# Kernel optimization log

Hardware: AMD Instinct MI355X
Metric: run time of the kernel (lower is better)

## Reference

```python
import jax, jax.numpy as jnp
import numpy as np

DIM = 1024
B, S = 4, 2048


def setup_inputs() -> dict:
    key = jax.random.key(0)
    kx, kq, kk, kv, ko = jax.random.split(key, 5)
    scale = 1.0 / np.sqrt(DIM)
    return {
        "x": jax.random.normal(kx, (B, S, DIM), dtype=jnp.float32),
        "wq": jax.random.normal(kq, (DIM, DIM), dtype=jnp.float32) * scale,
        "wk": jax.random.normal(kk, (DIM, DIM), dtype=jnp.float32) * scale,
        "wv": jax.random.normal(kv, (DIM, DIM), dtype=jnp.float32) * scale,
        "wo": jax.random.normal(ko, (DIM, DIM), dtype=jnp.float32) * scale,
    }


def reference(x, wq, wk, wv, wo):
    # nn.Linear(y) = y @ W.T ; weights stored [out, in]
    q = jnp.einsum("bsd,ed->bse", x, wq)
    k = jnp.einsum("bsd,ed->bse", x, wk)
    v = jnp.einsum("bsd,ed->bse", x, wv)
    # NOTE: no head split in original module; full-dim attention, scale = sqrt(dim)
    scores = jnp.einsum("bqd,bkd->bqk", q, k) / jnp.sqrt(jnp.float32(DIM))
    attn = jax.nn.softmax(scores, axis=-1)
    ctx = jnp.einsum("bqk,bkd->bqd", attn, v)
    return jnp.einsum("bsd,ed->bse", ctx, wo)
```

## Files before the change

### kernel.cpp

```cpp
#include <hip/hip_runtime.h>
#include <hip/hip_bf16.h>
#include <cstdio>
#include <cstdint>


typedef __attribute__((ext_vector_type(8))) short short8;
typedef __attribute__((ext_vector_type(4))) float f32x4;

#define AS1(p) ((const __attribute__((address_space(1))) void*)(p))
#define AS3(p) ((__attribute__((address_space(3))) void*)(p))

__device__ __forceinline__ unsigned short f2bf(float f) {
  union { float f; uint32_t u; } c; c.f = f;
  uint32_t u = c.u + 0x7fffu + ((c.u >> 16) & 1u);
  return (unsigned short)(u >> 16);
}

__global__ void cvt_f32_bf16(const float* __restrict__ in,
                             unsigned short* __restrict__ out, int n4) {
  int i = blockIdx.x * 256 + threadIdx.x;
  if (i >= n4) return;
  float4 v = ((const float4*)in)[i];
  ushort4 o;
  o.x = f2bf(v.x); o.y = f2bf(v.y); o.z = f2bf(v.z); o.w = f2bf(v.w);
  ((ushort4*)out)[i] = o;
}

__global__ void cvt_w4(const float* __restrict__ a, const float* __restrict__ b,
                       const float* __restrict__ c, const float* __restrict__ d,
                       unsigned short* __restrict__ out) {
  const float* s = (blockIdx.y == 0) ? a : (blockIdx.y == 1) ? b
                 : (blockIdx.y == 2) ? c : d;
  int i = blockIdx.x * 256 + threadIdx.x;
  float4 v = ((const float4*)s)[i];
  ushort4 o;
  o.x = f2bf(v.x); o.y = f2bf(v.y); o.z = f2bf(v.z); o.w = f2bf(v.w);
  ((ushort4*)(out + (size_t)blockIdx.y * 1048576))[i] = o;
}

__global__ void transpose_bf16(const unsigned short* __restrict__ V,
                               unsigned short* __restrict__ Vt) {
  __shared__ unsigned short tile[64][72];
  const int b = blockIdx.z;
  const unsigned short* v = V + (size_t)b * 2048 * 1024;
  unsigned short* vt = Vt + (size_t)b * 1024 * 2048;
  const int d0 = blockIdx.x * 64, s0 = blockIdx.y * 64;
  const int t = threadIdx.x;
#pragma unroll
  for (int it = 0; it < 16; ++it) {
    int idx = it * 256 + t, r = idx >> 6, c = idx & 63;
    tile[r][c] = v[(size_t)(s0 + r) * 1024 + d0 + c];
  }
  __syncthreads();
#pragma unroll
  for (int it = 0; it < 16; ++it) {
    int idx = it * 256 + t, r = idx >> 6, c = idx & 63;
    vt[(size_t)(d0 + r) * 2048 + s0 + c] = tile[c][r];
  }
}

__global__ void softmax_rows(const float* __restrict__ S,
                             unsigned short* __restrict__ P) {
  const size_t row = blockIdx.x;
  const float* s = S + row * 2048;
  const int t = threadIdx.x, l = t & 63, w = t >> 6;
  float4 v0 = ((const float4*)s)[t * 2];
  float4 v1 = ((const float4*)s)[t * 2 + 1];
  float x[8] = {v0.x, v0.y, v0.z, v0.w, v1.x, v1.y, v1.z, v1.w};
  float m = x[0];
#pragma unroll
  for (int j = 1; j < 8; ++j) m = fmaxf(m, x[j]);
#pragma unroll
  for (int d = 32; d; d >>= 1) m = fmaxf(m, __shfl_xor(m, d));
  __shared__ float rm[4], rs[4];
  if (l == 0) rm[w] = m;
  __syncthreads();
  m = fmaxf(fmaxf(rm[0], rm[1]), fmaxf(rm[2], rm[3]));
  float e[8], sum = 0.f;
#pragma unroll
  for (int j = 0; j < 8; ++j) { e[j] = __expf(x[j] - m); sum += e[j]; }
#pragma unroll
  for (int d = 32; d; d >>= 1) sum += __shfl_xor(sum, d);
  if (l == 0) rs[w] = sum;
  __syncthreads();
  float inv = 1.0f / (rs[0] + rs[1] + rs[2] + rs[3]);
  short8 o;
#pragma unroll
  for (int j = 0; j < 8; ++j) o[j] = (short)f2bf(e[j] * inv);
  *(short8*)(P + row * 2048 + t * 8) = o;
}

__device__ __forceinline__ void store_out(float* p, float v) { *p = v; }
__device__ __forceinline__ void store_out(unsigned short* p, float v) { *p = f2bf(v); }

template <typename OutT>
__global__ __launch_bounds__(512, 2) void gemm8p(
    const unsigned short* __restrict__ A, const unsigned short* __restrict__ B,
    OutT* __restrict__ C, int lda, int ldb, int ldc, int nT,
    long long aStride, long long bStride, long long cStride, float scale) {
  __shared__ unsigned short lds[65536];
  const int l = threadIdx.x & 63, w = threadIdx.x >> 6;
  const int wr = w >> 2, wc = w & 3;

  const int gx = gridDim.x, gy = gridDim.y;
  int f = blockIdx.x + gx * (blockIdx.y + gy * blockIdx.z);
  int nwg = gx * gy * gridDim.z;
  int work = ((nwg & 7) == 0) ? ((f & 7) * (nwg >> 3) + (f >> 3)) : f;
  const int bx = work % gx;
  int rem = work / gx;
  const int by = rem % gy, bz = rem / gy;
  const long long r0 = (long long)by * 256, c0 = (long long)bx * 256;
  A += (size_t)bz * aStride;
  B += (size_t)bz * bStride;
  C += (size_t)bz * cStride;

  const unsigned short* aS = A + (size_t)(r0 + w * 16 + (l & 15)) * lda + (l >> 4) * 8;
  const unsigned short* bS = B + (size_t)(c0 + w * 16 + (l & 15)) * ldb + (l >> 4) * 8;
  const size_t a128 = (size_t)128 * lda, b128 = (size_t)128 * ldb;
  char* const ldsc = (char*)lds;
  const int dstW = (w * 2) << 10;

#define STAGE_A(t_, h_)                                                        \
  do {                                                                         \
    const unsigned short* s_ = aS + ((h_) ? a128 : 0) + (t_) * 64;             \
    char* d_ = ldsc + (((t_) & 1) << 16) + ((h_) << 14) + dstW;                \
    __builtin_amdgcn_global_load_lds(AS1(s_), AS3(d_), 16, 0, 0);              \
    __builtin_amdgcn_global_load_lds(AS1(s_ + 32), AS3(d_ + 1024), 16, 0, 0);  \
  } while (0)
#define STAGE_B(t_, h_)                                                        \
  do {                                                                         \
    const unsigned short* s_ = bS + ((h_) ? b128 : 0) + (t_) * 64;             \
    char* d_ = ldsc + (((t_) & 1) << 16) + 32768 + ((h_) << 14) + dstW;        \
    __builtin_amdgcn_global_load_lds(AS1(s_), AS3(d_), 16, 0, 0);              \
    __builtin_amdgcn_global_load_lds(AS1(s_ + 32), AS3(d_ + 1024), 16, 0, 0);  \
  } while (0)

  short8 a[8], b0[4], b1[4];
  f32x4 acc[8][4] = {};

  const int aBase = wr << 14;
  const int bBase = 32768 + ((wc >> 1) << 14);
  const int bFr = (wc & 1) * 4;
  const int loff = l * 16;

#define LDA_SET(s_, qm_)                                                       \
  _Pragma("unroll") for (int m2 = 0; m2 < 4; ++m2)                             \
  _Pragma("unroll") for (int kk = 0; kk < 2; ++kk)                             \
      a[m2 * 2 + kk] = *(const short8*)(ldsc + ((s_) << 16) + aBase +          \
                                        ((((qm_) * 4 + m2) * 2 + kk) << 10) + loff);
#define LDB_SET(s_, qn_, dst_)                                                 \
  _Pragma("unroll") for (int n2 = 0; n2 < 2; ++n2)                             \
  _Pragma("unroll") for (int kk = 0; kk < 2; ++kk)                             \
      dst_[n2 * 2 + kk] = *(const short8*)(ldsc + ((s_) << 16) + bBase +       \
                                           (((bFr + (qn_) * 2 + n2) * 2 + kk) << 10) + loff);
#define MFMA_Q(qm_, qn_, bset_)                                                \
  __builtin_amdgcn_s_setprio(1);                                               \
  _Pragma("unroll") for (int m2 = 0; m2 < 4; ++m2)                             \
  _Pragma("unroll") for (int n2 = 0; n2 < 2; ++n2)                             \
  _Pragma("unroll") for (int kk = 0; kk < 2; ++kk)                             \
      acc[(qm_) * 4 + m2][(qn_) * 2 + n2] =                                    \
          __builtin_amdgcn_mfma_f32_16x16x32_bf16(                             \
              a[m2 * 2 + kk], bset_[n2 * 2 + kk],                              \
              acc[(qm_) * 4 + m2][(qn_) * 2 + n2], 0, 0, 0);                   \
  __builtin_amdgcn_s_setprio(0);
#define BAR() asm volatile("s_barrier" ::: "memory")
#define LGKM0() asm volatile("s_waitcnt lgkmcnt(0)" ::: "memory")
#define VMC(n_) asm volatile("s_waitcnt vmcnt(" #n_ ")" ::: "memory")

  STAGE_B(0, 0); STAGE_B(0, 1); STAGE_A(0, 0); STAGE_A(0, 1);
  STAGE_B(1, 0); STAGE_B(1, 1); STAGE_A(1, 0);
  VMC(6); BAR();

  const int nI = nT >> 1;
  for (int i = 0; i < nI; ++i) {
    const int t0 = 2 * i;
    const bool last = (i == nI - 1);
    LDA_SET(0, 0); LDB_SET(0, 0, b0);
    STAGE_A(t0 + 1, 1);
    BAR(); LGKM0(); MFMA_Q(0, 0, b0); BAR();
    LDB_SET(0, 1, b1);
    BAR(); LGKM0(); MFMA_Q(0, 1, b1); BAR();
    LDA_SET(0, 1);
    if (!last) STAGE_B(t0 + 2, 0);
    BAR(); LGKM0(); MFMA_Q(1, 1, b1); BAR();
    if (!last) { STAGE_B(t0 + 2, 1); VMC(4); } else { VMC(0); }
    BAR(); MFMA_Q(1, 0, b0); BAR();
    LDA_SET(1, 0); LDB_SET(1, 0, b0);
    if (!last) STAGE_A(t0 + 2, 0);
    BAR(); LGKM0(); MFMA_Q(0, 0, b0); BAR();
    LDB_SET(1, 1, b1);
    if (!last) STAGE_A(t0 + 2, 1);
    BAR(); LGKM0(); MFMA_Q(0, 1, b1); BAR();
    LDA_SET(1, 1);
    if (!last) STAGE_B(t0 + 3, 0);
    BAR(); LGKM0(); MFMA_Q(1, 1, b1); BAR();
    if (!last) { STAGE_B(t0 + 3, 1); STAGE_A(t0 + 3, 0); VMC(6); }
    BAR(); MFMA_Q(1, 0, b0); BAR();
  }
#undef STAGE_A
#undef STAGE_B
#undef LDA_SET
#undef LDB_SET
#undef MFMA_Q

  const int cr = (l >> 4) * 4, cc = l & 15;
  const long long rowb = r0 + wr * 128, colb = c0 + wc * 64;
#pragma unroll
  for (int m = 0; m < 8; ++m)
#pragma unroll
    for (int n = 0; n < 4; ++n) {
      long long col = colb + n * 16 + cc;
#pragma unroll
      for (int i2 = 0; i2 < 4; ++i2) {
        long long row = rowb + m * 16 + cr + i2;
        store_out(&C[row * ldc + col], acc[m][n][i2] * scale);
      }
    }
}

static const size_t OFF_XB  = 0;
static const size_t OFF_WQ  = 16777216;
static const size_t OFF_WK  = 18874368;
static const size_t OFF_WV  = 20971520;
static const size_t OFF_WO  = 23068672;
static const size_t OFF_Q   = 25165824;
static const size_t OFF_K   = 41943040;
static const size_t OFF_V   = 58720256;
static const size_t OFF_VT  = 75497472;
static const size_t OFF_SC  = 92274688;
static const size_t OFF_P   = 159383552;
static const size_t OFF_CTX = 192937984;
static const size_t WS_NEED = 209715200;

extern "C" void kernel_launch(void* const* d_in, const int* in_sizes, int n_in,
                              void* d_out, int out_size, void* d_ws, size_t ws_size,
                              hipStream_t stream) {
  const float* x  = (const float*)d_in[0];
  const float* wq = (const float*)d_in[1];
  const float* wk = (const float*)d_in[2];
  const float* wv = (const float*)d_in[3];
  const float* wo = (const float*)d_in[4];
  float* out = (float*)d_out;

  if (ws_size < WS_NEED) {
    fprintf(stderr, "kernel_launch: ws_size=%zu < needed %zu\n", ws_size, WS_NEED);
    return;
  }
  char* ws = (char*)d_ws;
  unsigned short* xb  = (unsigned short*)(ws + OFF_XB);
  unsigned short* wqb = (unsigned short*)(ws + OFF_WQ);
  unsigned short* wob = (unsigned short*)(ws + OFF_WO);
  unsigned short* Qb  = (unsigned short*)(ws + OFF_Q);
  unsigned short* Kb  = (unsigned short*)(ws + OFF_K);
  unsigned short* Vb  = (unsigned short*)(ws + OFF_V);
  unsigned short* Vt  = (unsigned short*)(ws + OFF_VT);
  float*          Sc  = (float*)(ws + OFF_SC);
  unsigned short* Pb  = (unsigned short*)(ws + OFF_P);
  unsigned short* Cx  = (unsigned short*)(ws + OFF_CTX);

  cvt_f32_bf16<<<8192, 256, 0, stream>>>(x, xb, 2097152);
  cvt_w4<<<dim3(1024, 4, 1), 256, 0, stream>>>(wq, wk, wv, wo, wqb);

  gemm8p<unsigned short><<<dim3(4, 32, 3), 512, 0, stream>>>(
      xb, wqb, Qb, 1024, 1024, 1024, 16, 0, 1048576LL, 8388608LL, 1.0f);

  transpose_bf16<<<dim3(16, 32, 4), 256, 0, stream>>>(Vb, Vt);

  gemm8p<float><<<dim3(8, 8, 4), 512, 0, stream>>>(
      Qb, Kb, Sc, 1024, 1024, 2048, 16,
      2097152LL, 2097152LL, 4194304LL, 0.03125f);

  softmax_rows<<<8192, 256, 0, stream>>>(Sc, Pb);

  gemm8p<unsigned short><<<dim3(4, 8, 4), 512, 0, stream>>>(
      Pb, Vt, Cx, 2048, 2048, 1024, 32,
      4194304LL, 2097152LL, 2097152LL, 1.0f);

  gemm8p<float><<<dim3(4, 32, 1), 512, 0, stream>>>(
      Cx, wob, out, 1024, 1024, 1024, 16, 0, 0, 0, 1.0f);
}
```

Measured before the change: 342.9 us.

## Restructure GEMM main loop with register double-buffered LDS reads and whole-tile staging

Rewrites the GEMM inner loop so LDS fragment reads for the next quarter-tile are issued before the current MFMA block, using separate even/odd A register sets and partial lgkmcnt waits instead of full waits. Global-to-LDS staging now loads a whole K-tile (A and B, both halves) at once into alternating slots, with fewer barriers per quarter. Sched barriers pin the ordering. This aims to hide LDS read latency behind MFMAs, at the cost of more registers and coarser global prefetch granularity.

```diff
diff --git a/kernel.cpp b/kernel.cpp
--- a/kernel.cpp
+++ b/kernel.cpp
@@ -94,7 +94,7 @@
 __device__ __forceinline__ void store_out(unsigned short* p, float v) { *p = f2bf(v); }
 
 template <typename OutT>
-__global__ __launch_bounds__(512, 2) void gemm8p(
+__global__ __launch_bounds__(512, 2) void gemm8w(
     const unsigned short* __restrict__ A, const unsigned short* __restrict__ B,
     OutT* __restrict__ C, int lda, int ldb, int ldc, int nT,
     long long aStride, long long bStride, long long cStride, float scale) {
@@ -119,89 +119,86 @@
   const size_t a128 = (size_t)128 * lda, b128 = (size_t)128 * ldb;
   char* const ldsc = (char*)lds;
   const int dstW = (w * 2) << 10;
-
-#define STAGE_A(t_, h_)                                                        \
-  do {                                                                         \
-    const unsigned short* s_ = aS + ((h_) ? a128 : 0) + (t_) * 64;             \
-    char* d_ = ldsc + (((t_) & 1) << 16) + ((h_) << 14) + dstW;                \
-    __builtin_amdgcn_global_load_lds(AS1(s_), AS3(d_), 16, 0, 0);              \
-    __builtin_amdgcn_global_load_lds(AS1(s_ + 32), AS3(d_ + 1024), 16, 0, 0);  \
-  } while (0)
-#define STAGE_B(t_, h_)                                                        \
-  do {                                                                         \
-    const unsigned short* s_ = bS + ((h_) ? b128 : 0) + (t_) * 64;             \
-    char* d_ = ldsc + (((t_) & 1) << 16) + 32768 + ((h_) << 14) + dstW;        \
-    __builtin_amdgcn_global_load_lds(AS1(s_), AS3(d_), 16, 0, 0);              \
-    __builtin_amdgcn_global_load_lds(AS1(s_ + 32), AS3(d_ + 1024), 16, 0, 0);  \
-  } while (0)
-
-  short8 a[8], b0[4], b1[4];
-  f32x4 acc[8][4] = {};
-
   const int aBase = wr << 14;
   const int bBase = 32768 + ((wc >> 1) << 14);
   const int bFr = (wc & 1) * 4;
   const int loff = l * 16;
 
-#define LDA_SET(s_, qm_)                                                       \
-  _Pragma("unroll") for (int m2 = 0; m2 < 4; ++m2)                             \
+#define STG(slot_, koff_)                                                      \
+  do {                                                                         \
+    const unsigned short* sa_ = aS + (koff_);                                  \
+    const unsigned short* sb_ = bS + (koff_);                                  \
+    char* da_ = ldsc + ((slot_) << 16) + dstW;                                 \
+    char* db_ = ldsc + ((slot_) << 16) + 32768 + dstW;                         \
+    __builtin_amdgcn_global_load_lds(AS1(sa_), AS3(da_), 16, 0, 0);            \
+    __builtin_amdgcn_global_load_lds(AS1(sa_ + 32), AS3(da_ + 1024), 16, 0, 0);\
+    __builtin_amdgcn_global_load_lds(AS1(sa_ + a128), AS3(da_ + 16384), 16, 0, 0);\
+    __builtin_amdgcn_global_load_lds(AS1(sa_ + a128 + 32), AS3(da_ + 17408), 16, 0, 0);\
+    __builtin_amdgcn_global_load_lds(AS1(sb_), AS3(db_), 16, 0, 0);            \
+    __builtin_amdgcn_global_load_lds(AS1(sb_ + 32), AS3(db_ + 1024), 16, 0, 0);\
+    __builtin_amdgcn_global_load_lds(AS1(sb_ + b128), AS3(db_ + 16384), 16, 0, 0);\
+    __builtin_amdgcn_global_load_lds(AS1(sb_ + b128 + 32), AS3(db_ + 17408), 16, 0, 0);\
+  } while (0)
+
+#define RDA(dst_, slot_, hs_)                                                  \
+  _Pragma("unroll") for (int f2 = 0; f2 < 4; ++f2)                             \
   _Pragma("unroll") for (int kk = 0; kk < 2; ++kk)                             \
-      a[m2 * 2 + kk] = *(const short8*)(ldsc + ((s_) << 16) + aBase +          \
-                                        ((((qm_) * 4 + m2) * 2 + kk) << 10) + loff);
-#define LDB_SET(s_, qn_, dst_)                                                 \
+      dst_[f2 * 2 + kk] = *(const short8*)(ldsc + ((slot_) << 16) + aBase +    \
+                                           ((((hs_) * 4 + f2) * 2 + kk) << 10) + loff);
+#define RDB(dst_, slot_, qn_)                                                  \
   _Pragma("unroll") for (int n2 = 0; n2 < 2; ++n2)                             \
   _Pragma("unroll") for (int kk = 0; kk < 2; ++kk)                             \
-      dst_[n2 * 2 + kk] = *(const short8*)(ldsc + ((s_) << 16) + bBase +       \
+      dst_[n2 * 2 + kk] = *(const short8*)(ldsc + ((slot_) << 16) + bBase +    \
                                            (((bFr + (qn_) * 2 + n2) * 2 + kk) << 10) + loff);
-#define MFMA_Q(qm_, qn_, bset_)                                                \
+#define MQ(ar_, mo_, br_, no_)                                                 \
   __builtin_amdgcn_s_setprio(1);                                               \
   _Pragma("unroll") for (int m2 = 0; m2 < 4; ++m2)                             \
   _Pragma("unroll") for (int n2 = 0; n2 < 2; ++n2)                             \
   _Pragma("unroll") for (int kk = 0; kk < 2; ++kk)                             \
-      acc[(qm_) * 4 + m2][(qn_) * 2 + n2] =                                    \
-          __builtin_amdgcn_mfma_f32_16x16x32_bf16(                             \
-              a[m2 * 2 + kk], bset_[n2 * 2 + kk],                              \
-              acc[(qm_) * 4 + m2][(qn_) * 2 + n2], 0, 0, 0);                   \
+      acc[(mo_) + m2][(no_) + n2] = __builtin_amdgcn_mfma_f32_16x16x32_bf16(   \
+          ar_[m2 * 2 + kk], br_[n2 * 2 + kk], acc[(mo_) + m2][(no_) + n2], 0, 0, 0); \
   __builtin_amdgcn_s_setprio(0);
 #define BAR() asm volatile("s_barrier" ::: "memory")
-#define LGKM0() asm volatile("s_waitcnt lgkmcnt(0)" ::: "memory")
+#define LGKM(n_) asm volatile("s_waitcnt lgkmcnt(" #n_ ")" ::: "memory")
 #define VMC(n_) asm volatile("s_waitcnt vmcnt(" #n_ ")" ::: "memory")
-
-  STAGE_B(0, 0); STAGE_B(0, 1); STAGE_A(0, 0); STAGE_A(0, 1);
-  STAGE_B(1, 0); STAGE_B(1, 1); STAGE_A(1, 0);
-  VMC(6); BAR();
+#define SB() __builtin_amdgcn_sched_barrier(0)
+
+  short8 aE[8], aO[8], b0r[4], b1r[4];
+  f32x4 acc[8][4] = {};
+
+  STG(0, 0);
+  STG(1, 64);
+  VMC(8); BAR();
+  RDA(aE, 0, 0);
+  RDB(b0r, 0, 0);
 
   const int nI = nT >> 1;
   for (int i = 0; i < nI; ++i) {
-    const int t0 = 2 * i;
     const bool last = (i == nI - 1);
-    LDA_SET(0, 0); LDB_SET(0, 0, b0);
-    STAGE_A(t0 + 1, 1);
-    BAR(); LGKM0(); MFMA_Q(0, 0, b0); BAR();
-    LDB_SET(0, 1, b1);
-    BAR(); LGKM0(); MFMA_Q(0, 1, b1); BAR();
-    LDA_SET(0, 1);
-    if (!last) STAGE_B(t0 + 2, 0);
-    BAR(); LGKM0(); MFMA_Q(1, 1, b1); BAR();
-    if (!last) { STAGE_B(t0 + 2, 1); VMC(4); } else { VMC(0); }
-    BAR(); MFMA_Q(1, 0, b0); BAR();
-    LDA_SET(1, 0); LDB_SET(1, 0, b0);
-    if (!last) STAGE_A(t0 + 2, 0);
-    BAR(); LGKM0(); MFMA_Q(0, 0, b0); BAR();
-    LDB_SET(1, 1, b1);
-    if (!last) STAGE_A(t0 + 2, 1);
-    BAR(); LGKM0(); MFMA_Q(0, 1, b1); BAR();
-    LDA_SET(1, 1);
-    if (!last) STAGE_B(t0 + 3, 0);
-    BAR(); LGKM0(); MFMA_Q(1, 1, b1); BAR();
-    if (!last) { STAGE_B(t0 + 3, 1); STAGE_A(t0 + 3, 0); VMC(6); }
-    BAR(); MFMA_Q(1, 0, b0); BAR();
-  }
-#undef STAGE_A
-#undef STAGE_B
-#undef LDA_SET
-#undef LDB_SET
-#undef MFMA_Q
+    RDB(b1r, 0, 1); LGKM(4); SB();
+    MQ(aE, 0, b0r, 0); BAR();
+    RDA(aO, 0, 1); LGKM(8); SB();
+    MQ(aE, 0, b1r, 2); VMC(0); BAR();
+    RDA(aE, 1, 0); LGKM(8); SB();
+    MQ(aO, 4, b0r, 0); BAR();
+    RDB(b0r, 1, 0);
+    if (!last) STG(0, 128);
+    MQ(aO, 4, b1r, 2); BAR();
+    RDB(b1r, 1, 1); LGKM(4); SB();
+    MQ(aE, 0, b0r, 0); BAR();
+    RDA(aO, 1, 1); LGKM(8); SB();
+    MQ(aE, 0, b1r, 2); VMC(0); BAR();
+    if (!last) { RDA(aE, 0, 0); LGKM(8); } else { LGKM(0); }
+    SB();
+    MQ(aO, 4, b0r, 0); BAR();
+    if (!last) { RDB(b0r, 0, 0); STG(1, 192); }
+    MQ(aO, 4, b1r, 2); BAR();
+    aS += 128; bS += 128;
+  }
+#undef STG
+#undef RDA
+#undef RDB
+#undef MQ
 
   const int cr = (l >> 4) * 4, cc = l & 15;
   const long long rowb = r0 + wr * 128, colb = c0 + wc * 64;
@@ -261,21 +258,21 @@
   cvt_f32_bf16<<<8192, 256, 0, stream>>>(x, xb, 2097152);
   cvt_w4<<<dim3(1024, 4, 1), 256, 0, stream>>>(wq, wk, wv, wo, wqb);
 
-  gemm8p<unsigned short><<<dim3(4, 32, 3), 512, 0, stream>>>(
+  gemm8w<unsigned short><<<dim3(4, 32, 3), 512, 0, stream>>>(
       xb, wqb, Qb, 1024, 1024, 1024, 16, 0, 1048576LL, 8388608LL, 1.0f);
 
   transpose_bf16<<<dim3(16, 32, 4), 256, 0, stream>>>(Vb, Vt);
 
-  gemm8p<float><<<dim3(8, 8, 4), 512, 0, stream>>>(
+  gemm8w<float><<<dim3(8, 8, 4), 512, 0, stream>>>(
       Qb, Kb, Sc, 1024, 1024, 2048, 16,
       2097152LL, 2097152LL, 4194304LL, 0.03125f);
 
   softmax_rows<<<8192, 256, 0, stream>>>(Sc, Pb);
 
-  gemm8p<unsigned short><<<dim3(4, 8, 4), 512, 0, stream>>>(
+  gemm8w<unsigned short><<<dim3(4, 8, 4), 512, 0, stream>>>(
       Pb, Vt, Cx, 2048, 2048, 1024, 32,
       4194304LL, 2097152LL, 2097152LL, 1.0f);
 
-  gemm8p<float><<<dim3(4, 32, 1), 512, 0, stream>>>(
+  gemm8w<float><<<dim3(4, 32, 1), 512, 0, stream>>>(
       Cx, wob, out, 1024, 1024, 1024, 16, 0, 0, 0, 1.0f);
 }
```

New measurement: 462.2 us. +34.8%, slower.
